# Kernel optimization log

Measured on AMD Instinct MI355X. Metric: run time of the kernel, lower is better.

## Reference

```python
import jax, jax.numpy as jnp
import numpy as np

N, E, D, H = 100000, 600000, 128, 128  # nodes, undirected edges, feat dim, mlp hidden


def setup_inputs() -> dict:
    key = jax.random.key(0)
    k = jax.random.split(key, 6)
    x = jax.random.normal(k[0], (N, D), dtype=jnp.float32)
    edge_attr = jax.random.normal(k[1], (E, D), dtype=jnp.float32)
    edge_index = jax.random.randint(k[2], (2, E), 0, N, dtype=jnp.int32)
    W1 = jax.random.normal(k[3], (D, H), dtype=jnp.float32) * (1.0 / np.sqrt(D))
    b1 = jnp.zeros((H,), dtype=jnp.float32)
    W2 = jax.random.normal(k[4], (H, D), dtype=jnp.float32) * (1.0 / np.sqrt(H))
    b2 = jnp.zeros((D,), dtype=jnp.float32)
    eps_node = jnp.zeros((1, 1), dtype=jnp.float32)  # trainable eps, init 0.0
    return {"x": x, "edge_attr": edge_attr, "W1": W1, "b1": b1,
            "W2": W2, "b2": b2, "eps_node": eps_node, "edge_index": edge_index}


def reference(x, edge_attr, W1, b1, W2, b2, eps_node, edge_index):
    # Per edge e=(u,v), the first-order edge tensor has 2 rows; after the
    # [1,0] swap, row at position u holds x[v] and row at position v holds x[u].
    # Adding repeat_interleave'd edge_attr and relu gives GINE messages.
    u, v = edge_index[0], edge_index[1]
    msg_to_u = jax.nn.relu(x[v] + edge_attr)  # [E, D]
    msg_to_v = jax.nn.relu(x[u] + edge_attr)  # [E, D]
    # gather edge->node (trivial subgraph): sum messages at each endpoint
    neighbor = jnp.zeros_like(x).at[u].add(msg_to_u).at[v].add(msg_to_v)
    h = (1.0 + eps_node) * x + neighbor  # eps-scaled residual combine
    h = jax.nn.relu(h @ W1 + b1)         # node MLP
    return h @ W2 + b2
```

## Files before the change

kernel.cpp:

```cpp
#include <hip/hip_runtime.h>

#define NN 100000
#define NE 600000
#define DD 128

#define WS_DEG      0
#define WS_PARTIALS 100352
#define WS_OFFS     100864
#define WS_CURSOR   201216
#define WS_ENTRIES  301568
#define ZERO_INTS   100864

__global__ __launch_bounds__(256) void zero_kernel(int* __restrict__ w) {
    const int i = blockIdx.x * 256 + threadIdx.x;
    if (i < ZERO_INTS) w[i] = 0;
}

__global__ __launch_bounds__(256) void hist_kernel(const int* __restrict__ ei,
                                                   int* __restrict__ deg) {
    const int e = blockIdx.x * 256 + threadIdx.x;
    if (e >= NE) return;
    atomicAdd(&deg[ei[e]], 1);
    atomicAdd(&deg[ei[NE + e]], 1);
}

__global__ __launch_bounds__(256) void scan1_kernel(const int* __restrict__ deg,
                                                    int* __restrict__ offs,
                                                    int* __restrict__ partials) {
    __shared__ int s[256];
    const int tid = threadIdx.x;
    const int i = blockIdx.x * 256 + tid;
    const int v = deg[i];
    s[tid] = v;
    __syncthreads();
#pragma unroll
    for (int d = 1; d < 256; d <<= 1) {
        const int t = (tid >= d) ? s[tid - d] : 0;
        __syncthreads();
        s[tid] += t;
        __syncthreads();
    }
    offs[i] = s[tid] - v;
    if (tid == 255) partials[blockIdx.x] = s[255];
}

__global__ __launch_bounds__(512) void scan2_kernel(int* __restrict__ partials) {
    __shared__ int s[512];
    const int tid = threadIdx.x;
    const int v = (tid < 391) ? partials[tid] : 0;
    s[tid] = v;
    __syncthreads();
#pragma unroll
    for (int d = 1; d < 512; d <<= 1) {
        const int t = (tid >= d) ? s[tid - d] : 0;
        __syncthreads();
        s[tid] += t;
        __syncthreads();
    }
    if (tid < 391) partials[tid] = s[tid] - v;
    __syncthreads();
}

__global__ __launch_bounds__(256) void finalize_kernel(int* __restrict__ offs,
                                                       const int* __restrict__ partials,
                                                       int* __restrict__ cursor) {
    const int i = blockIdx.x * 256 + threadIdx.x;
    if (i > NN) return;
    const int r = offs[i] + partials[i >> 8];
    offs[i] = r;
    if (i < NN) cursor[i] = r;
}

__global__ __launch_bounds__(256) void fill_kernel(const int* __restrict__ ei,
                                                   int* __restrict__ cursor,
                                                   int* __restrict__ entries) {
    const int e = blockIdx.x * 256 + threadIdx.x;
    if (e >= NE) return;
    const int u = ei[e];
    const int v = ei[NE + e];
    const int p1 = atomicAdd(&cursor[u], 1);
    entries[p1] = (e << 1);
    const int p2 = atomicAdd(&cursor[v], 1);
    entries[p2] = (e << 1) | 1;
}

__global__ __launch_bounds__(256) void init_kernel(const float* __restrict__ x,
                                                   const float* __restrict__ eps_p,
                                                   float* __restrict__ out) {
    const int i = blockIdx.x * 256 + threadIdx.x;
    const float s = 1.0f + eps_p[0];
    float4 v = reinterpret_cast<const float4*>(x)[i];
    v.x *= s; v.y *= s; v.z *= s; v.w *= s;
    reinterpret_cast<float4*>(out)[i] = v;
}

__global__ __launch_bounds__(256) void gather_kernel(const float* __restrict__ x,
                                                     const float* __restrict__ ea,
                                                     const int* __restrict__ ei,
                                                     const int* __restrict__ offs,
                                                     const int* __restrict__ entries,
                                                     float* __restrict__ out) {
    const int node = blockIdx.x * 8 + (threadIdx.x >> 5);
    const int t = threadIdx.x & 31;
    const int start = offs[node];
    const int end = offs[node + 1];
    const float4* x4 = reinterpret_cast<const float4*>(x);
    const float4* ea4 = reinterpret_cast<const float4*>(ea);
    float4 acc = {0.0f, 0.0f, 0.0f, 0.0f};
    for (int j = start; j < end; ++j) {
        const int entry = entries[j];
        const int e = entry >> 1;
        const int other = (entry & 1) ? ei[e] : ei[NE + e];
        const float4 a = ea4[(size_t)e * 32 + t];
        const float4 xo = x4[(size_t)other * 32 + t];
        acc.x += fmaxf(xo.x + a.x, 0.0f);
        acc.y += fmaxf(xo.y + a.y, 0.0f);
        acc.z += fmaxf(xo.z + a.z, 0.0f);
        acc.w += fmaxf(xo.w + a.w, 0.0f);
    }
    float4* out4 = reinterpret_cast<float4*>(out);
    const size_t oi = (size_t)node * 32 + t;
    float4 o = out4[oi];
    o.x += acc.x; o.y += acc.y; o.z += acc.z; o.w += acc.w;
    out4[oi] = o;
}

template <int RELU>
__global__ __launch_bounds__(256) void mlp_kernel(const float* __restrict__ in,
                                                  const float* __restrict__ W,
                                                  const float* __restrict__ bias,
                                                  float* __restrict__ out) {
    __shared__ float Wl[DD * DD];
    __shared__ float hl[32 * DD];
    const int tid = threadIdx.x;
    float4* Wl4 = reinterpret_cast<float4*>(Wl);
    const float4* W4 = reinterpret_cast<const float4*>(W);
#pragma unroll
    for (int i = 0; i < 16; ++i) Wl4[i * 256 + tid] = W4[i * 256 + tid];

    const int base = blockIdx.x * 32;
    float4* hl4 = reinterpret_cast<float4*>(hl);
    const float4* in4 = reinterpret_cast<const float4*>(in);
#pragma unroll
    for (int i = 0; i < 4; ++i)
        hl4[i * 256 + tid] = in4[(size_t)base * 32 + i * 256 + tid];
    __syncthreads();

    const int g = tid >> 5;
    const int t = tid & 31;
    const float4* h0 = reinterpret_cast<const float4*>(hl + (4 * g + 0) * DD);
    const float4* h1 = reinterpret_cast<const float4*>(hl + (4 * g + 1) * DD);
    const float4* h2 = reinterpret_cast<const float4*>(hl + (4 * g + 2) * DD);
    const float4* h3 = reinterpret_cast<const float4*>(hl + (4 * g + 3) * DD);

    float4 acc0 = {0, 0, 0, 0}, acc1 = {0, 0, 0, 0};
    float4 acc2 = {0, 0, 0, 0}, acc3 = {0, 0, 0, 0};

#pragma unroll 8
    for (int kq = 0; kq < 32; ++kq) {
        const float4 ha = h0[kq];
        const float4 hb = h1[kq];
        const float4 hc = h2[kq];
        const float4 hd = h3[kq];
        const float4 w0 = Wl4[(4 * kq + 0) * 32 + t];
        const float4 w1 = Wl4[(4 * kq + 1) * 32 + t];
        const float4 w2 = Wl4[(4 * kq + 2) * 32 + t];
        const float4 w3 = Wl4[(4 * kq + 3) * 32 + t];

#define ACC_STEP(A, H)                                    \
        A.x = fmaf(H.x, w0.x, A.x);                       \
        A.y = fmaf(H.x, w0.y, A.y);                       \
        A.z = fmaf(H.x, w0.z, A.z);                       \
        A.w = fmaf(H.x, w0.w, A.w);                       \
        A.x = fmaf(H.y, w1.x, A.x);                       \
        A.y = fmaf(H.y, w1.y, A.y);                       \
        A.z = fmaf(H.y, w1.z, A.z);                       \
        A.w = fmaf(H.y, w1.w, A.w);                       \
        A.x = fmaf(H.z, w2.x, A.x);                       \
        A.y = fmaf(H.z, w2.y, A.y);                       \
        A.z = fmaf(H.z, w2.z, A.z);                       \
        A.w = fmaf(H.z, w2.w, A.w);                       \
        A.x = fmaf(H.w, w3.x, A.x);                       \
        A.y = fmaf(H.w, w3.y, A.y);                       \
        A.z = fmaf(H.w, w3.z, A.z);                       \
        A.w = fmaf(H.w, w3.w, A.w);
        ACC_STEP(acc0, ha)
        ACC_STEP(acc1, hb)
        ACC_STEP(acc2, hc)
        ACC_STEP(acc3, hd)
#undef ACC_STEP
    }

    const float4 bb = reinterpret_cast<const float4*>(bias)[t];
    acc0.x += bb.x; acc0.y += bb.y; acc0.z += bb.z; acc0.w += bb.w;
    acc1.x += bb.x; acc1.y += bb.y; acc1.z += bb.z; acc1.w += bb.w;
    acc2.x += bb.x; acc2.y += bb.y; acc2.z += bb.z; acc2.w += bb.w;
    acc3.x += bb.x; acc3.y += bb.y; acc3.z += bb.z; acc3.w += bb.w;
    if (RELU) {
        acc0.x = fmaxf(acc0.x, 0.0f); acc0.y = fmaxf(acc0.y, 0.0f);
        acc0.z = fmaxf(acc0.z, 0.0f); acc0.w = fmaxf(acc0.w, 0.0f);
        acc1.x = fmaxf(acc1.x, 0.0f); acc1.y = fmaxf(acc1.y, 0.0f);
        acc1.z = fmaxf(acc1.z, 0.0f); acc1.w = fmaxf(acc1.w, 0.0f);
        acc2.x = fmaxf(acc2.x, 0.0f); acc2.y = fmaxf(acc2.y, 0.0f);
        acc2.z = fmaxf(acc2.z, 0.0f); acc2.w = fmaxf(acc2.w, 0.0f);
        acc3.x = fmaxf(acc3.x, 0.0f); acc3.y = fmaxf(acc3.y, 0.0f);
        acc3.z = fmaxf(acc3.z, 0.0f); acc3.w = fmaxf(acc3.w, 0.0f);
    }

    float4* out4 = reinterpret_cast<float4*>(out);
    const size_t n0 = (size_t)(base + 4 * g) * 32 + t;
    out4[n0 + 0 * 32] = acc0;
    out4[n0 + 1 * 32] = acc1;
    out4[n0 + 2 * 32] = acc2;
    out4[n0 + 3 * 32] = acc3;
}

extern "C" void kernel_launch(void* const* d_in, const int* in_sizes, int n_in,
                              void* d_out, int out_size, void* d_ws, size_t ws_size,
                              hipStream_t stream) {
    const float* x    = (const float*)d_in[0];
    const float* ea   = (const float*)d_in[1];
    const float* W1   = (const float*)d_in[2];
    const float* b1   = (const float*)d_in[3];
    const float* W2   = (const float*)d_in[4];
    const float* b2   = (const float*)d_in[5];
    const float* eps  = (const float*)d_in[6];
    const int*   ei   = (const int*)d_in[7];
    float* out = (float*)d_out;

    int* w        = (int*)d_ws;
    int* deg      = w + WS_DEG;
    int* partials = w + WS_PARTIALS;
    int* offs     = w + WS_OFFS;
    int* cursor   = w + WS_CURSOR;
    int* entries  = w + WS_ENTRIES;

    zero_kernel<<<(ZERO_INTS + 255) / 256, 256, 0, stream>>>(w);
    hist_kernel<<<(NE + 255) / 256, 256, 0, stream>>>(ei, deg);
    scan1_kernel<<<391, 256, 0, stream>>>(deg, offs, partials);
    scan2_kernel<<<1, 512, 0, stream>>>(partials);
    finalize_kernel<<<391, 256, 0, stream>>>(offs, partials, cursor);
    fill_kernel<<<(NE + 255) / 256, 256, 0, stream>>>(ei, cursor, entries);

    init_kernel<<<NN * DD / 4 / 256, 256, 0, stream>>>(x, eps, out);
    gather_kernel<<<NN / 8, 256, 0, stream>>>(x, ea, ei, offs, entries, out);
    mlp_kernel<1><<<NN / 32, 256, 0, stream>>>(out, W1, b1, out);
    mlp_kernel<0><<<NN / 32, 256, 0, stream>>>(out, W2, b2, out);
}
```

Measured before the change: 893.7 us.

## Store neighbor id in CSR entries, unroll gather by two, persistent MLP grid

The CSR fill now stores (edge, other-node) pairs, so the gather no longer makes a dependent lookup into edge_index for each neighbor. The gather loop is unrolled by two so that more independent loads are in flight per iteration. The MLP kernels become persistent with 512 blocks, loading the weight matrix into shared memory once per block instead of once per 32-row tile. In exchange the entries array doubles in size, and fewer MLP blocks may limit occupancy and latency hiding.

```diff
diff --git a/kernel.cpp b/kernel.cpp
--- a/kernel.cpp
+++ b/kernel.cpp
@@ -58,7 +58,6 @@
         __syncthreads();
     }
     if (tid < 391) partials[tid] = s[tid] - v;
-    __syncthreads();
 }
 
 __global__ __launch_bounds__(256) void finalize_kernel(int* __restrict__ offs,
@@ -73,15 +72,15 @@
 
 __global__ __launch_bounds__(256) void fill_kernel(const int* __restrict__ ei,
                                                    int* __restrict__ cursor,
-                                                   int* __restrict__ entries) {
+                                                   int2* __restrict__ entries2) {
     const int e = blockIdx.x * 256 + threadIdx.x;
     if (e >= NE) return;
     const int u = ei[e];
     const int v = ei[NE + e];
     const int p1 = atomicAdd(&cursor[u], 1);
-    entries[p1] = (e << 1);
+    entries2[p1] = make_int2(e, v);
     const int p2 = atomicAdd(&cursor[v], 1);
-    entries[p2] = (e << 1) | 1;
+    entries2[p2] = make_int2(e, u);
 }
 
 __global__ __launch_bounds__(256) void init_kernel(const float* __restrict__ x,
@@ -96,9 +95,8 @@
 
 __global__ __launch_bounds__(256) void gather_kernel(const float* __restrict__ x,
                                                      const float* __restrict__ ea,
-                                                     const int* __restrict__ ei,
                                                      const int* __restrict__ offs,
-                                                     const int* __restrict__ entries,
+                                                     const int2* __restrict__ entries2,
                                                      float* __restrict__ out) {
     const int node = blockIdx.x * 8 + (threadIdx.x >> 5);
     const int t = threadIdx.x & 31;
@@ -107,16 +105,27 @@
     const float4* x4 = reinterpret_cast<const float4*>(x);
     const float4* ea4 = reinterpret_cast<const float4*>(ea);
     float4 acc = {0.0f, 0.0f, 0.0f, 0.0f};
-    for (int j = start; j < end; ++j) {
-        const int entry = entries[j];
-        const int e = entry >> 1;
-        const int other = (entry & 1) ? ei[e] : ei[NE + e];
-        const float4 a = ea4[(size_t)e * 32 + t];
-        const float4 xo = x4[(size_t)other * 32 + t];
-        acc.x += fmaxf(xo.x + a.x, 0.0f);
-        acc.y += fmaxf(xo.y + a.y, 0.0f);
-        acc.z += fmaxf(xo.z + a.z, 0.0f);
-        acc.w += fmaxf(xo.w + a.w, 0.0f);
+    int j = start;
+    for (; j + 1 < end; j += 2) {
+        const int2 p0 = entries2[j];
+        const int2 p1 = entries2[j + 1];
+        const float4 a0 = ea4[(size_t)p0.x * 32 + t];
+        const float4 x0 = x4[(size_t)p0.y * 32 + t];
+        const float4 a1 = ea4[(size_t)p1.x * 32 + t];
+        const float4 x1 = x4[(size_t)p1.y * 32 + t];
+        acc.x += fmaxf(x0.x + a0.x, 0.0f) + fmaxf(x1.x + a1.x, 0.0f);
+        acc.y += fmaxf(x0.y + a0.y, 0.0f) + fmaxf(x1.y + a1.y, 0.0f);
+        acc.z += fmaxf(x0.z + a0.z, 0.0f) + fmaxf(x1.z + a1.z, 0.0f);
+        acc.w += fmaxf(x0.w + a0.w, 0.0f) + fmaxf(x1.w + a1.w, 0.0f);
+    }
+    if (j < end) {
+        const int2 p0 = entries2[j];
+        const float4 a0 = ea4[(size_t)p0.x * 32 + t];
+        const float4 x0 = x4[(size_t)p0.y * 32 + t];
+        acc.x += fmaxf(x0.x + a0.x, 0.0f);
+        acc.y += fmaxf(x0.y + a0.y, 0.0f);
+        acc.z += fmaxf(x0.z + a0.z, 0.0f);
+        acc.w += fmaxf(x0.w + a0.w, 0.0f);
     }
     float4* out4 = reinterpret_cast<float4*>(out);
     const size_t oi = (size_t)node * 32 + t;
@@ -124,6 +133,9 @@
     o.x += acc.x; o.y += acc.y; o.z += acc.z; o.w += acc.w;
     out4[oi] = o;
 }
+
+#define MLP_GRID 512
+#define NTILES   (NN / 32)
 
 template <int RELU>
 __global__ __launch_bounds__(256) void mlp_kernel(const float* __restrict__ in,
@@ -138,81 +150,85 @@
 #pragma unroll
     for (int i = 0; i < 16; ++i) Wl4[i * 256 + tid] = W4[i * 256 + tid];
 
-    const int base = blockIdx.x * 32;
+    const int g = tid >> 5;
+    const int t = tid & 31;
+    const float4 bb = reinterpret_cast<const float4*>(bias)[t];
     float4* hl4 = reinterpret_cast<float4*>(hl);
     const float4* in4 = reinterpret_cast<const float4*>(in);
-#pragma unroll
-    for (int i = 0; i < 4; ++i)
-        hl4[i * 256 + tid] = in4[(size_t)base * 32 + i * 256 + tid];
-    __syncthreads();
-
-    const int g = tid >> 5;
-    const int t = tid & 31;
-    const float4* h0 = reinterpret_cast<const float4*>(hl + (4 * g + 0) * DD);
-    const float4* h1 = reinterpret_cast<const float4*>(hl + (4 * g + 1) * DD);
-    const float4* h2 = reinterpret_cast<const float4*>(hl + (4 * g + 2) * DD);
-    const float4* h3 = reinterpret_cast<const float4*>(hl + (4 * g + 3) * DD);
-
-    float4 acc0 = {0, 0, 0, 0}, acc1 = {0, 0, 0, 0};
-    float4 acc2 = {0, 0, 0, 0}, acc3 = {0, 0, 0, 0};
+    float4* out4 = reinterpret_cast<float4*>(out);
+
+    for (int tile = blockIdx.x; tile < NTILES; tile += MLP_GRID) {
+        const int base = tile * 32;
+        __syncthreads();
+#pragma unroll
+        for (int i = 0; i < 4; ++i)
+            hl4[i * 256 + tid] = in4[(size_t)base * 32 + i * 256 + tid];
+        __syncthreads();
+
+        const float4* h0 = reinterpret_cast<const float4*>(hl + (4 * g + 0) * DD);
+        const float4* h1 = reinterpret_cast<const float4*>(hl + (4 * g + 1) * DD);
+        const float4* h2 = reinterpret_cast<const float4*>(hl + (4 * g + 2) * DD);
+        const float4* h3 = reinterpret_cast<const float4*>(hl + (4 * g + 3) * DD);
+
+        float4 acc0 = {0, 0, 0, 0}, acc1 = {0, 0, 0, 0};
+        float4 acc2 = {0, 0, 0, 0}, acc3 = {0, 0, 0, 0};
 
 #pragma unroll 8
-    for (int kq = 0; kq < 32; ++kq) {
-        const float4 ha = h0[kq];
-        const float4 hb = h1[kq];
-        const float4 hc = h2[kq];
-        const float4 hd = h3[kq];
-        const float4 w0 = Wl4[(4 * kq + 0) * 32 + t];
-        const float4 w1 = Wl4[(4 * kq + 1) * 32 + t];
-        const float4 w2 = Wl4[(4 * kq + 2) * 32 + t];
-        const float4 w3 = Wl4[(4 * kq + 3) * 32 + t];
+        for (int kq = 0; kq < 32; ++kq) {
+            const float4 ha = h0[kq];
+            const float4 hb = h1[kq];
+            const float4 hc = h2[kq];
+            const float4 hd = h3[kq];
+            const float4 w0 = Wl4[(4 * kq + 0) * 32 + t];
+            const float4 w1 = Wl4[(4 * kq + 1) * 32 + t];
+            const float4 w2 = Wl4[(4 * kq + 2) * 32 + t];
+            const float4 w3 = Wl4[(4 * kq + 3) * 32 + t];
 
 #define ACC_STEP(A, H)                                    \
-        A.x = fmaf(H.x, w0.x, A.x);                       \
-        A.y = fmaf(H.x, w0.y, A.y);                       \
-        A.z = fmaf(H.x, w0.z, A.z);                       \
-        A.w = fmaf(H.x, w0.w, A.w);                       \
-        A.x = fmaf(H.y, w1.x, A.x);                       \
-        A.y = fmaf(H.y, w1.y, A.y);                       \
-        A.z = fmaf(H.y, w1.z, A.z);                       \
-        A.w = fmaf(H.y, w1.w, A.w);                       \
-        A.x = fmaf(H.z, w2.x, A.x);                       \
-        A.y = fmaf(H.z, w2.y, A.y);                       \
-        A.z = fmaf(H.z, w2.z, A.z);                       \
-        A.w = fmaf(H.z, w2.w, A.w);                       \
-        A.x = fmaf(H.w, w3.x, A.x);                       \
-        A.y = fmaf(H.w, w3.y, A.y);                       \
-        A.z = fmaf(H.w, w3.z, A.z);                       \
-        A.w = fmaf(H.w, w3.w, A.w);
-        ACC_STEP(acc0, ha)
-        ACC_STEP(acc1, hb)
-        ACC_STEP(acc2, hc)
-        ACC_STEP(acc3, hd)
+            A.x = fmaf(H.x, w0.x, A.x);                   \
+            A.y = fmaf(H.x, w0.y, A.y);                   \
+            A.z = fmaf(H.x, w0.z, A.z);                   \
+            A.w = fmaf(H.x, w0.w, A.w);                   \
+            A.x = fmaf(H.y, w1.x, A.x);                   \
+            A.y = fmaf(H.y, w1.y, A.y);                   \
+            A.z = fmaf(H.y, w1.z, A.z);                   \
+            A.w = fmaf(H.y, w1.w, A.w);                   \
+            A.x = fmaf(H.z, w2.x, A.x);                   \
+            A.y = fmaf(H.z, w2.y, A.y);                   \
+            A.z = fmaf(H.z, w2.z, A.z);                   \
+            A.w = fmaf(H.z, w2.w, A.w);                   \
+            A.x = fmaf(H.w, w3.x, A.x);                   \
+            A.y = fmaf(H.w, w3.y, A.y);                   \
+            A.z = fmaf(H.w, w3.z, A.z);                   \
+            A.w = fmaf(H.w, w3.w, A.w);
+            ACC_STEP(acc0, ha)
+            ACC_STEP(acc1, hb)
+            ACC_STEP(acc2, hc)
+            ACC_STEP(acc3, hd)
 #undef ACC_STEP
-    }
-
-    const float4 bb = reinterpret_cast<const float4*>(bias)[t];
-    acc0.x += bb.x; acc0.y += bb.y; acc0.z += bb.z; acc0.w += bb.w;
-    acc1.x += bb.x; acc1.y += bb.y; acc1.z += bb.z; acc1.w += bb.w;
-    acc2.x += bb.x; acc2.y += bb.y; acc2.z += bb.z; acc2.w += bb.w;
-    acc3.x += bb.x; acc3.y += bb.y; acc3.z += bb.z; acc3.w += bb.w;
-    if (RELU) {
-        acc0.x = fmaxf(acc0.x, 0.0f); acc0.y = fmaxf(acc0.y, 0.0f);
-        acc0.z = fmaxf(acc0.z, 0.0f); acc0.w = fmaxf(acc0.w, 0.0f);
-        acc1.x = fmaxf(acc1.x, 0.0f); acc1.y = fmaxf(acc1.y, 0.0f);
-        acc1.z = fmaxf(acc1.z, 0.0f); acc1.w = fmaxf(acc1.w, 0.0f);
-        acc2.x = fmaxf(acc2.x, 0.0f); acc2.y = fmaxf(acc2.y, 0.0f);
-        acc2.z = fmaxf(acc2.z, 0.0f); acc2.w = fmaxf(acc2.w, 0.0f);
-        acc3.x = fmaxf(acc3.x, 0.0f); acc3.y = fmaxf(acc3.y, 0.0f);
-        acc3.z = fmaxf(acc3.z, 0.0f); acc3.w = fmaxf(acc3.w, 0.0f);
-    }
-
-    float4* out4 = reinterpret_cast<float4*>(out);
-    const size_t n0 = (size_t)(base + 4 * g) * 32 + t;
-    out4[n0 + 0 * 32] = acc0;
-    out4[n0 + 1 * 32] = acc1;
-    out4[n0 + 2 * 32] = acc2;
-    out4[n0 + 3 * 32] = acc3;
+        }
+
+        acc0.x += bb.x; acc0.y += bb.y; acc0.z += bb.z; acc0.w += bb.w;
+        acc1.x += bb.x; acc1.y += bb.y; acc1.z += bb.z; acc1.w += bb.w;
+        acc2.x += bb.x; acc2.y += bb.y; acc2.z += bb.z; acc2.w += bb.w;
+        acc3.x += bb.x; acc3.y += bb.y; acc3.z += bb.z; acc3.w += bb.w;
+        if (RELU) {
+            acc0.x = fmaxf(acc0.x, 0.0f); acc0.y = fmaxf(acc0.y, 0.0f);
+            acc0.z = fmaxf(acc0.z, 0.0f); acc0.w = fmaxf(acc0.w, 0.0f);
+            acc1.x = fmaxf(acc1.x, 0.0f); acc1.y = fmaxf(acc1.y, 0.0f);
+            acc1.z = fmaxf(acc1.z, 0.0f); acc1.w = fmaxf(acc1.w, 0.0f);
+            acc2.x = fmaxf(acc2.x, 0.0f); acc2.y = fmaxf(acc2.y, 0.0f);
+            acc2.z = fmaxf(acc2.z, 0.0f); acc2.w = fmaxf(acc2.w, 0.0f);
+            acc3.x = fmaxf(acc3.x, 0.0f); acc3.y = fmaxf(acc3.y, 0.0f);
+            acc3.z = fmaxf(acc3.z, 0.0f); acc3.w = fmaxf(acc3.w, 0.0f);
+        }
+
+        const size_t n0 = (size_t)(base + 4 * g) * 32 + t;
+        out4[n0 + 0 * 32] = acc0;
+        out4[n0 + 1 * 32] = acc1;
+        out4[n0 + 2 * 32] = acc2;
+        out4[n0 + 3 * 32] = acc3;
+    }
 }
 
 extern "C" void kernel_launch(void* const* d_in, const int* in_sizes, int n_in,
@@ -228,22 +244,22 @@
     const int*   ei   = (const int*)d_in[7];
     float* out = (float*)d_out;
 
-    int* w        = (int*)d_ws;
-    int* deg      = w + WS_DEG;
-    int* partials = w + WS_PARTIALS;
-    int* offs     = w + WS_OFFS;
-    int* cursor   = w + WS_CURSOR;
-    int* entries  = w + WS_ENTRIES;
+    int*  w        = (int*)d_ws;
+    int*  deg      = w + WS_DEG;
+    int*  partials = w + WS_PARTIALS;
+    int*  offs     = w + WS_OFFS;
+    int*  cursor   = w + WS_CURSOR;
+    int2* entries2 = (int2*)(w + WS_ENTRIES);
 
     zero_kernel<<<(ZERO_INTS + 255) / 256, 256, 0, stream>>>(w);
     hist_kernel<<<(NE + 255) / 256, 256, 0, stream>>>(ei, deg);
     scan1_kernel<<<391, 256, 0, stream>>>(deg, offs, partials);
     scan2_kernel<<<1, 512, 0, stream>>>(partials);
     finalize_kernel<<<391, 256, 0, stream>>>(offs, partials, cursor);
-    fill_kernel<<<(NE + 255) / 256, 256, 0, stream>>>(ei, cursor, entries);
+    fill_kernel<<<(NE + 255) / 256, 256, 0, stream>>>(ei, cursor, entries2);
 
     init_kernel<<<NN * DD / 4 / 256, 256, 0, stream>>>(x, eps, out);
-    gather_kernel<<<NN / 8, 256, 0, stream>>>(x, ea, ei, offs, entries, out);
-    mlp_kernel<1><<<NN / 32, 256, 0, stream>>>(out, W1, b1, out);
-    mlp_kernel<0><<<NN / 32, 256, 0, stream>>>(out, W2, b2, out);
-}
+    gather_kernel<<<NN / 8, 256, 0, stream>>>(x, ea, offs, entries2, out);
+    mlp_kernel<1><<<MLP_GRID, 256, 0, stream>>>(out, W1, b1, out);
+    mlp_kernel<0><<<MLP_GRID, 256, 0, stream>>>(out, W2, b2, out);
+}
```

Result: faster. 807.5 us (-9.6%).
